# Performance work log

Measured on AMD Instinct MI355X. Metric: run time of the kernel, lower is better.

The kernel has to match this reference:

```python
import jax, jax.numpy as jnp
import numpy as np


def _normalized_adj(A):
    # get_a: d = 0.5*I, a = off-diagonal ones + A, a2 = d @ a @ d
    off = jnp.array([[0., 1., 1.], [1., 0., 1.], [1., 1., 0.]], dtype=A.dtype)
    a = off + A
    d = 0.5 * jnp.eye(3, dtype=A.dtype)
    return d @ a @ d  # [3,3]


def setup_inputs() -> dict:
    key = jax.random.key(0)
    k1, k2 = jax.random.split(key)
    B = 8192
    x = jax.random.normal(k1, (B, 3, 10), dtype=jnp.float32)
    A = jnp.eye(3, dtype=jnp.float32)  # get_A() returns identity; Parameter init
    stdv = 1.0 / np.sqrt(10.0)
    W = jax.random.uniform(k2, (10, 10), dtype=jnp.float32, minval=-stdv, maxval=stdv)
    return {"x": x, "A": A, "W": W}


def reference(x, A, W):
    # adjacency is detached in the torch forward
    adj = jax.lax.stop_gradient(_normalized_adj(A))  # [3,3], shared across batch
    # GraphConvolution: adj @ (x @ W)
    support = jnp.einsum('bnf,fo->bno', x, W)          # [B,3,10]
    h = jnp.einsum('nm,bmo->bno', adj, support)        # [B,3,10]
    # permute -> [B,10,3]; AvgPool1d(2) on length 3 -> length 1: mean of nodes 0,1
    pooled = 0.5 * (h[:, 0, :] + h[:, 1, :])           # [B,10]
    # ScaleDotProductAttention over the batch axis
    score = jax.nn.softmax(pooled @ pooled.T, axis=-1)  # [B,B]
    v = score @ pooled                                  # [B,10]
    return v
```

## Files before the change

kernel.cpp:

```cpp
#include <hip/hip_runtime.h>
#include <math.h>

#define BROWS 8192
#define F 10
#define TJ 512
#define QP 20
#define AP 524
#define NT (BROWS / TJ)
#define LOG2E 1.44269504088896340736f

#if __has_builtin(__builtin_amdgcn_exp2f)
#define EXP2F(x) __builtin_amdgcn_exp2f(x)
#else
#define EXP2F(x) exp2f(x)
#endif

typedef _Float16 half4 __attribute__((ext_vector_type(4)));
typedef __fp16 fp16x2 __attribute__((ext_vector_type(2)));
typedef float floatx4 __attribute__((ext_vector_type(4)));

__device__ __forceinline__ half4 exp4_to_h4(float a, float b, float c, float d) {
#if __has_builtin(__builtin_amdgcn_cvt_pkrtz)
    union { fp16x2 h2[2]; half4 h4; } u;
    u.h2[0] = __builtin_amdgcn_cvt_pkrtz(EXP2F(a), EXP2F(b));
    u.h2[1] = __builtin_amdgcn_cvt_pkrtz(EXP2F(c), EXP2F(d));
    return u.h4;
#else
    half4 r;
    r[0] = (_Float16)EXP2F(a); r[1] = (_Float16)EXP2F(b);
    r[2] = (_Float16)EXP2F(c); r[3] = (_Float16)EXP2F(d);
    return r;
#endif
}

__device__ __forceinline__ uint32_t pack2(_Float16 a, _Float16 b) {
    union { _Float16 h[2]; uint32_t u; } x;
    x.h[0] = a; x.h[1] = b;
    return x.u;
}

__device__ __forceinline__ void gload_lds16(const void* g, void* l) {
#if __has_builtin(__builtin_amdgcn_global_load_lds)
    __builtin_amdgcn_global_load_lds(
        (const __attribute__((address_space(1))) void*)g,
        (__attribute__((address_space(3))) void*)l, 16, 0, 0);
#else
    *(float4*)l = *(const float4*)g;
#endif
}

__global__ void pooled_kernel(const float* __restrict__ x,
                              const float* __restrict__ A,
                              const float* __restrict__ W,
                              _Float16* __restrict__ poolQ,
                              _Float16* __restrict__ poolT16) {
    int b = blockIdx.x * blockDim.x + threadIdx.x;
    if (b >= BROWS) return;

    float c0 = 0.125f * (1.0f + A[0] + A[3]);
    float c1 = 0.125f * (1.0f + A[1] + A[4]);
    float c2 = 0.125f * (2.0f + A[2] + A[5]);

    const float2* xb = (const float2*)(x + (size_t)b * 3 * F);
    float xv[3 * F];
#pragma unroll
    for (int k = 0; k < 15; ++k) {
        float2 t = xb[k];
        xv[2 * k] = t.x; xv[2 * k + 1] = t.y;
    }

    float y[F];
#pragma unroll
    for (int f = 0; f < F; ++f)
        y[f] = c0 * xv[f] + c1 * xv[F + f] + c2 * xv[2 * F + f];

    float po[F];
#pragma unroll
    for (int o = 0; o < F; ++o) {
        float acc = 0.0f;
#pragma unroll
        for (int f = 0; f < F; ++f)
            acc = fmaf(y[f], W[f * F + o], acc);
        po[o] = acc;
    }

    uint2* qd = (uint2*)(poolQ + (size_t)b * QP);
    qd[0] = make_uint2(pack2((_Float16)po[0], (_Float16)po[1]),
                       pack2((_Float16)po[2], (_Float16)po[3]));
    qd[1] = make_uint2(pack2((_Float16)po[4], (_Float16)po[5]),
                       pack2((_Float16)po[6], (_Float16)po[7]));
    qd[2] = make_uint2(pack2((_Float16)po[8], (_Float16)po[9]), 0u);
    qd[3] = make_uint2(0u, 0u);
    qd[4] = make_uint2(0u, 0u);

#pragma unroll
    for (int o = 0; o < F; ++o)
        poolT16[(size_t)o * BROWS + b] = (_Float16)po[o];
    poolT16[(size_t)10 * BROWS + b] = (_Float16)1.0f;
#pragma unroll
    for (int o = 11; o < 16; ++o)
        poolT16[(size_t)o * BROWS + b] = (_Float16)0.0f;
}

__global__ void attn_kernel(const _Float16* __restrict__ poolQ,
                            const _Float16* __restrict__ poolT16,
                            float* __restrict__ out) {
    __shared__ __align__(16) _Float16 qbuf[2][TJ * QP];
    __shared__ __align__(16) _Float16 abuf[2][16 * AP];
    float* red = (float*)&qbuf[0][0];

    const int tid  = threadIdx.x;
    const int wave = tid >> 6;
    const int lane = tid & 63;
    const int m    = lane & 15;
    const int quad = lane >> 4;
    const int irow = blockIdx.x * 16 + m;

    half4 b1;
#pragma unroll
    for (int idx = 0; idx < 4; ++idx) {
        int f = quad * 4 + idx;
        float v = (f < F) ? (float)poolQ[(size_t)irow * QP + f] * LOG2E : 0.0f;
        b1[idx] = (_Float16)v;
    }

    auto dma_tile = [&](int t, int bufi) {
        const char* qs = (const char*)poolQ + (size_t)t * TJ * QP * 2;
        char* qd = (char*)&qbuf[bufi][0];
        for (int d = wave; d < 20; d += 8)
            gload_lds16(qs + d * 1024 + lane * 16, qd + d * 1024 + lane * 16);
        char* ad = (char*)&abuf[bufi][0];
        for (int n = wave; n < 16; n += 8)
            gload_lds16((const char*)(poolT16 + (size_t)n * BROWS + t * TJ) + lane * 16,
                        ad + n * (AP * 2) + lane * 16);
    };

    floatx4 acc0 = {0.f, 0.f, 0.f, 0.f};
    floatx4 acc1 = {0.f, 0.f, 0.f, 0.f};

    dma_tile(0, 0);
    __syncthreads();

    for (int t = 0; t < NT; ++t) {
        const int buf = t & 1;
        if (t + 1 < NT) dma_tile(t + 1, buf ^ 1);

#pragma unroll
        for (int c = 0; c < 4; ++c) {
            const int jb = wave * 64 + c * 16;
            half4 ag = *(const half4*)&abuf[buf][m * AP + jb + quad * 4];
            half4 a1 = *(const half4*)&qbuf[buf][(jb + m) * QP + quad * 4];
            floatx4 d1 = __builtin_amdgcn_mfma_f32_16x16x16f16(
                a1, b1, (floatx4){0.f, 0.f, 0.f, 0.f}, 0, 0, 0);
            half4 a2 = exp4_to_h4(d1[0], d1[1], d1[2], d1[3]);
            if (c & 1)
                acc1 = __builtin_amdgcn_mfma_f32_16x16x16f16(ag, a2, acc1, 0, 0, 0);
            else
                acc0 = __builtin_amdgcn_mfma_f32_16x16x16f16(ag, a2, acc0, 0, 0, 0);
        }
        __syncthreads();
    }

    floatx4 acc = acc0 + acc1;

    if (quad < 3)
        *(floatx4*)&red[(wave * 16 + m) * 12 + quad * 4] = acc;
    __syncthreads();

    if (tid < 160) {
        const int i16 = tid / 10;
        const int f   = tid % 10;
        float sum = 0.0f, l = 0.0f;
#pragma unroll
        for (int w = 0; w < 8; ++w) {
            sum += red[(w * 16 + i16) * 12 + f];
            l   += red[(w * 16 + i16) * 12 + 10];
        }
        out[(size_t)(blockIdx.x * 16 + i16) * F + f] = sum / l;
    }
}

extern "C" void kernel_launch(void* const* d_in, const int* in_sizes, int n_in,
                              void* d_out, int out_size, void* d_ws, size_t ws_size,
                              hipStream_t stream) {
    const float* x = (const float*)d_in[0];
    const float* A = (const float*)d_in[1];
    const float* W = (const float*)d_in[2];
    float* out = (float*)d_out;

    _Float16* poolQ   = (_Float16*)d_ws;
    _Float16* poolT16 = (_Float16*)((char*)d_ws + 327680);

    pooled_kernel<<<BROWS / 64, 64, 0, stream>>>(x, A, W, poolQ, poolT16);
    attn_kernel<<<BROWS / 16, 512, 0, stream>>>(poolQ, poolT16, out);
}
```

Baseline: 75.50 us.

## Process 32 query rows per block with 16 waves to reuse key tiles

Each attention block now handles 32 query rows instead of 16, using two B-fragments per wave and 16 waves of 64 threads. Each wave covers 32 key columns per tile instead of 64. Every key/value tile staged into LDS is reused across twice as many queries, which halves global-to-LDS traffic per row and gives each wave two independent MFMA chains for more instruction-level parallelism. In exchange the grid drops to 256 blocks of 1024 threads, which changes occupancy and per-CU load balance, and the final reduction sums over 16 waves instead of 8.

```diff
diff --git a/kernel.cpp b/kernel.cpp
--- a/kernel.cpp
+++ b/kernel.cpp
@@ -7,6 +7,8 @@
 #define QP 20
 #define AP 524
 #define NT (BROWS / TJ)
+#define IB 32
+#define NW 16
 #define LOG2E 1.44269504088896340736f
 
 #if __has_builtin(__builtin_amdgcn_exp2f)
@@ -114,29 +116,33 @@
     const int lane = tid & 63;
     const int m    = lane & 15;
     const int quad = lane >> 4;
-    const int irow = blockIdx.x * 16 + m;
-
-    half4 b1;
+    const int i0   = blockIdx.x * IB;
+
+    half4 b1a, b1b;
 #pragma unroll
     for (int idx = 0; idx < 4; ++idx) {
         int f = quad * 4 + idx;
-        float v = (f < F) ? (float)poolQ[(size_t)irow * QP + f] * LOG2E : 0.0f;
-        b1[idx] = (_Float16)v;
+        float va = (f < F) ? (float)poolQ[(size_t)(i0 + m) * QP + f] * LOG2E : 0.0f;
+        float vb = (f < F) ? (float)poolQ[(size_t)(i0 + 16 + m) * QP + f] * LOG2E : 0.0f;
+        b1a[idx] = (_Float16)va;
+        b1b[idx] = (_Float16)vb;
     }
 
     auto dma_tile = [&](int t, int bufi) {
         const char* qs = (const char*)poolQ + (size_t)t * TJ * QP * 2;
         char* qd = (char*)&qbuf[bufi][0];
-        for (int d = wave; d < 20; d += 8)
+        for (int d = wave; d < 20; d += NW)
             gload_lds16(qs + d * 1024 + lane * 16, qd + d * 1024 + lane * 16);
         char* ad = (char*)&abuf[bufi][0];
-        for (int n = wave; n < 16; n += 8)
+        {
+            const int n = wave;
             gload_lds16((const char*)(poolT16 + (size_t)n * BROWS + t * TJ) + lane * 16,
                         ad + n * (AP * 2) + lane * 16);
+        }
     };
 
-    floatx4 acc0 = {0.f, 0.f, 0.f, 0.f};
-    floatx4 acc1 = {0.f, 0.f, 0.f, 0.f};
+    floatx4 accA0 = {0.f,0.f,0.f,0.f}, accA1 = {0.f,0.f,0.f,0.f};
+    floatx4 accB0 = {0.f,0.f,0.f,0.f}, accB1 = {0.f,0.f,0.f,0.f};
 
     dma_tile(0, 0);
     __syncthreads();
@@ -146,37 +152,46 @@
         if (t + 1 < NT) dma_tile(t + 1, buf ^ 1);
 
 #pragma unroll
-        for (int c = 0; c < 4; ++c) {
-            const int jb = wave * 64 + c * 16;
+        for (int c = 0; c < 2; ++c) {
+            const int jb = wave * 32 + c * 16;
             half4 ag = *(const half4*)&abuf[buf][m * AP + jb + quad * 4];
             half4 a1 = *(const half4*)&qbuf[buf][(jb + m) * QP + quad * 4];
-            floatx4 d1 = __builtin_amdgcn_mfma_f32_16x16x16f16(
-                a1, b1, (floatx4){0.f, 0.f, 0.f, 0.f}, 0, 0, 0);
-            half4 a2 = exp4_to_h4(d1[0], d1[1], d1[2], d1[3]);
-            if (c & 1)
-                acc1 = __builtin_amdgcn_mfma_f32_16x16x16f16(ag, a2, acc1, 0, 0, 0);
-            else
-                acc0 = __builtin_amdgcn_mfma_f32_16x16x16f16(ag, a2, acc0, 0, 0, 0);
+            floatx4 d1a = __builtin_amdgcn_mfma_f32_16x16x16f16(
+                a1, b1a, (floatx4){0.f,0.f,0.f,0.f}, 0, 0, 0);
+            floatx4 d1b = __builtin_amdgcn_mfma_f32_16x16x16f16(
+                a1, b1b, (floatx4){0.f,0.f,0.f,0.f}, 0, 0, 0);
+            half4 a2a = exp4_to_h4(d1a[0], d1a[1], d1a[2], d1a[3]);
+            half4 a2b = exp4_to_h4(d1b[0], d1b[1], d1b[2], d1b[3]);
+            if (c) {
+                accA1 = __builtin_amdgcn_mfma_f32_16x16x16f16(ag, a2a, accA1, 0, 0, 0);
+                accB1 = __builtin_amdgcn_mfma_f32_16x16x16f16(ag, a2b, accB1, 0, 0, 0);
+            } else {
+                accA0 = __builtin_amdgcn_mfma_f32_16x16x16f16(ag, a2a, accA0, 0, 0, 0);
+                accB0 = __builtin_amdgcn_mfma_f32_16x16x16f16(ag, a2b, accB0, 0, 0, 0);
+            }
         }
         __syncthreads();
     }
 
-    floatx4 acc = acc0 + acc1;
-
-    if (quad < 3)
-        *(floatx4*)&red[(wave * 16 + m) * 12 + quad * 4] = acc;
+    floatx4 accA = accA0 + accA1;
+    floatx4 accB = accB0 + accB1;
+
+    if (quad < 3) {
+        *(floatx4*)&red[((size_t)wave * IB + m) * 12 + quad * 4] = accA;
+        *(floatx4*)&red[((size_t)wave * IB + 16 + m) * 12 + quad * 4] = accB;
+    }
     __syncthreads();
 
-    if (tid < 160) {
-        const int i16 = tid / 10;
-        const int f   = tid % 10;
+    if (tid < IB * F) {
+        const int i = tid / F;
+        const int f = tid % F;
         float sum = 0.0f, l = 0.0f;
 #pragma unroll
-        for (int w = 0; w < 8; ++w) {
-            sum += red[(w * 16 + i16) * 12 + f];
-            l   += red[(w * 16 + i16) * 12 + 10];
+        for (int w = 0; w < NW; ++w) {
+            sum += red[((size_t)w * IB + i) * 12 + f];
+            l   += red[((size_t)w * IB + i) * 12 + 10];
         }
-        out[(size_t)(blockIdx.x * 16 + i16) * F + f] = sum / l;
+        out[(size_t)(i0 + i) * F + f] = sum / l;
     }
 }
 
@@ -192,5 +207,5 @@
     _Float16* poolT16 = (_Float16*)((char*)d_ws + 327680);
 
     pooled_kernel<<<BROWS / 64, 64, 0, stream>>>(x, A, W, poolQ, poolT16);
-    attn_kernel<<<BROWS / 16, 512, 0, stream>>>(poolQ, poolT16, out);
-}
+    attn_kernel<<<BROWS / IB, NW * 64, 0, stream>>>(poolQ, poolT16, out);
+}
```

New measurement: 75.95 us. No clear change (+0.6%).
